# Optimization experiments

Measured on AMD Instinct MI355X. Metric: run time of the kernel, lower is better.

Reference implementation:

```python
import jax, jax.numpy as jnp
import numpy as np

T = 100000   # total firing-model timesteps (undefined global `time` in source; chosen)
WARM = 200   # warm-start rows (time_fomer = data[0:200, :])
N = 69       # neurons
EPS = 1e-5   # torch BatchNorm default eps


def _conv_same(x, w):
    # torch conv2d_same_padding with k=4, stride=1: F.pad([0,1,0,1]) then conv padding=1
    # => asymmetric SAME padding (1,2) on each spatial dim, output H,W preserved.
    return jax.lax.conv_general_dilated(
        x, w, (1, 1), [(1, 2), (1, 2)],
        dimension_numbers=('NCHW', 'OIHW', 'NCHW'))


def _up2(x):
    # nearest-neighbor upsample x2 (F.upsample(size=2*H, mode='nearest'))
    return jnp.repeat(jnp.repeat(x, 2, axis=2), 2, axis=3)


def _bn(x, g, b):
    # BatchNorm2d in training mode: batch statistics over (N,H,W), biased variance.
    m = x.mean(axis=(0, 2, 3), keepdims=True)
    v = x.var(axis=(0, 2, 3), keepdims=True)
    return (x - m) * jax.lax.rsqrt(v + EPS) * g[None, :, None, None] + b[None, :, None, None]


def _forward(x, start_part, W_in, b_in, w1, w2, w3, w4, w5,
             g1, be1, g2, be2, g3, be3, g4, be4, W_d2, b_d2):
    h = x @ W_in.T + b_in                                   # (1, 12800)
    h = h.reshape(-1, 512, 5, 5)
    h = jax.nn.relu(_bn(_conv_same(_up2(h), w1), g1, be1))  # (1,512,10,10)
    h = jax.nn.relu(_bn(_conv_same(_up2(h), w2), g2, be2))  # (1,256,20,20)
    h = jax.nn.relu(_bn(_conv_same(_up2(h), w3), g3, be3))  # (1,128,40,40)
    h = jax.nn.relu(_bn(_conv_same(_up2(h), w4), g4, be4))  # (1,64,80,80)
    h = jnp.tanh(_conv_same(h, w5))                         # (1,1,80,80)
    h = h.reshape(80 * 80) @ W_d2.T + b_d2                  # (4761,)
    w = h.reshape(N, N)                                     # coupling matrix

    # spiking recurrence: spike[t, i] = -spike[t-1, i] + tanh(sum_j w[j, i] * spike[t-1, j])
    def step(prev, _):
        new = -prev + jnp.tanh(prev @ w)                    # (69,)
        return new, new

    _, rows = jax.lax.scan(step, start_part[-1], None, length=T - WARM)
    return rows[None]                                       # (1, T-200, 69)


def setup_inputs() -> dict:
    key = jax.random.key(0)
    ks = jax.random.split(key, 9)
    f32 = jnp.float32
    return {
        'x': jax.random.normal(ks[0], (1, 2048), f32),
        'start_part': jax.random.normal(ks[1], (WARM, N), f32),
        'W_in': jax.random.normal(ks[2], (12800, 2048), f32) * (2048.0 ** -0.5),
        'b_in': jnp.zeros((12800,), f32),
        'w1': jax.random.uniform(ks[3], (512, 512, 4, 4), f32),
        'w2': jax.random.uniform(ks[4], (256, 512, 4, 4), f32),
        'w3': jax.random.uniform(ks[5], (128, 256, 4, 4), f32),
        'w4': jax.random.uniform(ks[6], (64, 128, 4, 4), f32),
        'w5': jax.random.uniform(ks[7], (1, 64, 4, 4), f32),
        'g1': jnp.ones((512,), f32), 'be1': jnp.zeros((512,), f32),
        'g2': jnp.ones((256,), f32), 'be2': jnp.zeros((256,), f32),
        'g3': jnp.ones((128,), f32), 'be3': jnp.zeros((128,), f32),
        'g4': jnp.ones((64,), f32), 'be4': jnp.zeros((64,), f32),
        'W_d2': jax.random.normal(ks[8], (4761, 6400), f32) * (6400.0 ** -0.5),
        'b_d2': jnp.zeros((4761,), f32),
    }


def reference(x, start_part, W_in, b_in, w1, w2, w3, w4, w5,
              g1, be1, g2, be2, g3, be3, g4, be4, W_d2, b_d2):
    return _forward(x, start_part, W_in, b_in, w1, w2, w3, w4, w5,
                    g1, be1, g2, be2, g3, be3, g4, be4, W_d2, b_d2)
```

## Files before the change

### kernel.cpp

```cpp
#include <hip/hip_runtime.h>
#include <cstddef>
#include <cstdint>

__global__ void fc1_k(const float* __restrict__ W, const float* __restrict__ x,
                      const float* __restrict__ b, float* __restrict__ y,
                      int rows, int cols) {
  int wave = threadIdx.x >> 6, lane = threadIdx.x & 63;
  int r = blockIdx.x * 4 + wave;
  if (r >= rows) return;
  const float* wp = W + (size_t)r * cols;
  float s = 0.f;
  for (int j = lane; j < cols; j += 64) s = fmaf(wp[j], x[j], s);
  for (int o = 32; o; o >>= 1) s += __shfl_down(s, o);
  if (lane == 0) y[r] = s + b[r];
}

template <int UP>
__global__ void conv_k(const float* __restrict__ in, const float* __restrict__ wt,
                       float* __restrict__ out, int Cin, int Cout, int OH, int OW,
                       int Hin, int Win) {
  int idx = blockIdx.x * blockDim.x + threadIdx.x;
  int total = Cout * OH * OW;
  if (idx >= total) return;
  int ox = idx % OW;
  int tt = idx / OW;
  int oy = tt % OH;
  int co = tt / OH;
  const float* wco = wt + (size_t)co * Cin * 16;
  float acc = 0.f;
  for (int ci = 0; ci < Cin; ++ci) {
    const float* ip = in + (size_t)ci * Hin * Win;
    const float* wp = wco + ci * 16;
#pragma unroll
    for (int ky = 0; ky < 4; ++ky) {
      int iy = oy - 1 + ky;
      if ((unsigned)iy >= (unsigned)OH) continue;
      int sy = UP ? (iy >> 1) : iy;
      const float* iprow = ip + sy * Win;
#pragma unroll
      for (int kx = 0; kx < 4; ++kx) {
        int ix = ox - 1 + kx;
        if ((unsigned)ix >= (unsigned)OW) continue;
        int sx = UP ? (ix >> 1) : ix;
        acc = fmaf(iprow[sx], wp[ky * 4 + kx], acc);
      }
    }
  }
  out[idx] = acc;
}

__global__ void stats_k(const float* __restrict__ x, float* __restrict__ mean,
                        float* __restrict__ rstd, int HW) {
  int c = blockIdx.x;
  const float* p = x + (size_t)c * HW;
  double s = 0.0, s2 = 0.0;
  for (int i = threadIdx.x; i < HW; i += blockDim.x) {
    float v = p[i];
    s += v;
    s2 += (double)v * (double)v;
  }
  for (int o = 32; o; o >>= 1) {
    s += __shfl_down(s, o);
    s2 += __shfl_down(s2, o);
  }
  __shared__ double sh[2][4];
  int wv = threadIdx.x >> 6, ln = threadIdx.x & 63;
  if (ln == 0) { sh[0][wv] = s; sh[1][wv] = s2; }
  __syncthreads();
  if (threadIdx.x == 0) {
    double S = 0, S2 = 0;
    int nw = blockDim.x >> 6;
    for (int w = 0; w < nw; ++w) { S += sh[0][w]; S2 += sh[1][w]; }
    double m = S / HW;
    double v = S2 / HW - m * m;
    if (v < 0) v = 0;
    mean[c] = (float)m;
    rstd[c] = rsqrtf((float)v + 1e-5f);
  }
}

__global__ void bnrelu_k(float* __restrict__ x, const float* __restrict__ mean,
                         const float* __restrict__ rstd, const float* __restrict__ g,
                         const float* __restrict__ be, int HW, int total) {
  int idx = blockIdx.x * blockDim.x + threadIdx.x;
  if (idx >= total) return;
  int c = idx / HW;
  float v = (x[idx] - mean[c]) * rstd[c] * g[c] + be[c];
  x[idx] = v > 0.f ? v : 0.f;
}

__global__ void tanh_k(float* __restrict__ x, int n) {
  int i = blockIdx.x * blockDim.x + threadIdx.x;
  if (i < n) x[i] = tanhf(x[i]);
}

__global__ void fc2_k(const float* __restrict__ W, const float* __restrict__ h,
                      const float* __restrict__ b, float* __restrict__ y, int cols) {
  int r = blockIdx.x;
  const float* wp = W + (size_t)r * cols;
  float s = 0.f;
  for (int j = threadIdx.x; j < cols; j += blockDim.x) s = fmaf(wp[j], h[j], s);
  for (int o = 32; o; o >>= 1) s += __shfl_down(s, o);
  __shared__ float sh[4];
  int wv = threadIdx.x >> 6, ln = threadIdx.x & 63;
  if (ln == 0) sh[wv] = s;
  __syncthreads();
  if (threadIdx.x == 0) y[r] = sh[0] + sh[1] + sh[2] + sh[3] + b[r];
}

__global__ __launch_bounds__(320, 1) void scan_k(const float* __restrict__ wmat,
                                                 const float* __restrict__ start,
                                                 float* __restrict__ out, int steps) {
  const int t = threadIdx.x;
  const int i = t >> 2;
  const int k = t & 3;
  float wr[20];
#pragma unroll
  for (int m = 0; m < 20; ++m) {
    int j = 20 * k + m;
    wr[m] = (i < 69 && j < 69) ? wmat[(size_t)j * 69 + i] : 0.f;
  }
  __shared__ __align__(16) float pbuf[2][80];
  if (t < 80) {
    pbuf[0][t] = (t < 69) ? start[t] : 0.f;
    pbuf[1][t] = 0.f;
  }
  __syncthreads();
  int p = 0;
  for (int step = 0; step < steps; ++step) {
    const float* pv = pbuf[p];
    const float4* q = reinterpret_cast<const float4*>(pv) + 5 * k;
    float4 q0 = q[0], q1 = q[1], q2 = q[2], q3 = q[3], q4 = q[4];
    float prev_i = pv[i];
    float a0 = q0.x * wr[0];
    float a1 = q0.y * wr[1];
    float a2 = q0.z * wr[2];
    float a3 = q0.w * wr[3];
    a0 = fmaf(q1.x, wr[4], a0);
    a1 = fmaf(q1.y, wr[5], a1);
    a2 = fmaf(q1.z, wr[6], a2);
    a3 = fmaf(q1.w, wr[7], a3);
    a0 = fmaf(q2.x, wr[8], a0);
    a1 = fmaf(q2.y, wr[9], a1);
    a2 = fmaf(q2.z, wr[10], a2);
    a3 = fmaf(q2.w, wr[11], a3);
    a0 = fmaf(q3.x, wr[12], a0);
    a1 = fmaf(q3.y, wr[13], a1);
    a2 = fmaf(q3.z, wr[14], a2);
    a3 = fmaf(q3.w, wr[15], a3);
    a0 = fmaf(q4.x, wr[16], a0);
    a1 = fmaf(q4.y, wr[17], a1);
    a2 = fmaf(q4.z, wr[18], a2);
    a3 = fmaf(q4.w, wr[19], a3);
    float s = (a0 + a1) + (a2 + a3);
    s += __shfl_xor(s, 1);
    s += __shfl_xor(s, 2);
    float e = __expf(2.f * s);
    float th = 1.f - __fdividef(2.f, e + 1.f);
    float nv = th - prev_i;
    if (i < 69) {
      if (k == 0) pbuf[p ^ 1][i] = nv;
      else if (k == 1) out[(size_t)step * 69 + i] = nv;
    }
    __syncthreads();
    p ^= 1;
  }
}

extern "C" void kernel_launch(void* const* d_in, const int* in_sizes, int n_in,
                              void* d_out, int out_size, void* d_ws, size_t ws_size,
                              hipStream_t stream) {
  const float* x    = (const float*)d_in[0];
  const float* strt = (const float*)d_in[1];
  const float* W_in = (const float*)d_in[2];
  const float* b_in = (const float*)d_in[3];
  const float* w1   = (const float*)d_in[4];
  const float* w2   = (const float*)d_in[5];
  const float* w3   = (const float*)d_in[6];
  const float* w4   = (const float*)d_in[7];
  const float* w5   = (const float*)d_in[8];
  const float* g1   = (const float*)d_in[9];
  const float* be1  = (const float*)d_in[10];
  const float* g2   = (const float*)d_in[11];
  const float* be2  = (const float*)d_in[12];
  const float* g3   = (const float*)d_in[13];
  const float* be3  = (const float*)d_in[14];
  const float* g4   = (const float*)d_in[15];
  const float* be4  = (const float*)d_in[16];
  const float* W_d2 = (const float*)d_in[17];
  const float* b_d2 = (const float*)d_in[18];
  float* out = (float*)d_out;

  float* ws   = (float*)d_ws;
  float* fc1  = ws;
  float* A    = ws + 16384;
  float* B    = A + 204800;
  float* mean = B + 409600;
  float* rstd = mean + 512;
  float* wmat = rstd + 512;

  fc1_k<<<12800 / 4, 256, 0, stream>>>(W_in, x, b_in, fc1, 12800, 2048);

  conv_k<1><<<(512 * 100 + 255) / 256, 256, 0, stream>>>(fc1, w1, A, 512, 512, 10, 10, 5, 5);
  stats_k<<<512, 256, 0, stream>>>(A, mean, rstd, 100);
  bnrelu_k<<<(51200 + 255) / 256, 256, 0, stream>>>(A, mean, rstd, g1, be1, 100, 51200);

  conv_k<1><<<(256 * 400 + 255) / 256, 256, 0, stream>>>(A, w2, B, 512, 256, 20, 20, 10, 10);
  stats_k<<<256, 256, 0, stream>>>(B, mean, rstd, 400);
  bnrelu_k<<<(102400 + 255) / 256, 256, 0, stream>>>(B, mean, rstd, g2, be2, 400, 102400);

  conv_k<1><<<(128 * 1600 + 255) / 256, 256, 0, stream>>>(B, w3, A, 256, 128, 40, 40, 20, 20);
  stats_k<<<128, 256, 0, stream>>>(A, mean, rstd, 1600);
  bnrelu_k<<<(204800 + 255) / 256, 256, 0, stream>>>(A, mean, rstd, g3, be3, 1600, 204800);

  conv_k<1><<<(64 * 6400 + 255) / 256, 256, 0, stream>>>(A, w4, B, 128, 64, 80, 80, 40, 40);
  stats_k<<<64, 256, 0, stream>>>(B, mean, rstd, 6400);
  bnrelu_k<<<(409600 + 255) / 256, 256, 0, stream>>>(B, mean, rstd, g4, be4, 6400, 409600);

  conv_k<0><<<(6400 + 255) / 256, 256, 0, stream>>>(B, w5, A, 64, 1, 80, 80, 80, 80);
  tanh_k<<<(6400 + 255) / 256, 256, 0, stream>>>(A, 6400);

  fc2_k<<<4761, 256, 0, stream>>>(W_d2, A, b_d2, wmat, 6400);

  scan_k<<<1, 320, 0, stream>>>(wmat, strt + 199 * 69, out, 99800);
}
```

Measured before the change: 36.70 ms.

## Run spiking recurrence in a single wavefront using readlane broadcasts

The sequential scan moves from a 320-thread block, which exchanged state through shared memory and needed __syncthreads each step, to a single 64-lane wavefront. Each lane holds two columns of the coupling matrix in registers (138 floats). The previous state vector is broadcast with readlane, so the per-step barrier, LDS round trip and cross-lane reduction are gone. The cost is 138 serial FMAs per lane per step instead of about 20, plus high register pressure that could spill.

```diff
diff --git a/kernel.cpp b/kernel.cpp
--- a/kernel.cpp
+++ b/kernel.cpp
@@ -108,62 +108,53 @@
   if (threadIdx.x == 0) y[r] = sh[0] + sh[1] + sh[2] + sh[3] + b[r];
 }
 
-__global__ __launch_bounds__(320, 1) void scan_k(const float* __restrict__ wmat,
-                                                 const float* __restrict__ start,
-                                                 float* __restrict__ out, int steps) {
-  const int t = threadIdx.x;
-  const int i = t >> 2;
-  const int k = t & 3;
-  float wr[20];
-#pragma unroll
-  for (int m = 0; m < 20; ++m) {
-    int j = 20 * k + m;
-    wr[m] = (i < 69 && j < 69) ? wmat[(size_t)j * 69 + i] : 0.f;
-  }
-  __shared__ __align__(16) float pbuf[2][80];
-  if (t < 80) {
-    pbuf[0][t] = (t < 69) ? start[t] : 0.f;
-    pbuf[1][t] = 0.f;
-  }
-  __syncthreads();
-  int p = 0;
+__global__ __launch_bounds__(64, 1) void scan_k(const float* __restrict__ wmat,
+                                                const float* __restrict__ start,
+                                                float* __restrict__ out, int steps) {
+  const int l = threadIdx.x;
+  const int sec = (l < 5) ? 64 + l : l;
+
+  float2 wp[69];
+#pragma unroll
+  for (int j = 0; j < 69; ++j) {
+    wp[j].x = wmat[j * 69 + l];
+    wp[j].y = wmat[j * 69 + sec];
+  }
+
+  float2 p;
+  p.x = start[l];
+  p.y = start[sec];
+
   for (int step = 0; step < steps; ++step) {
-    const float* pv = pbuf[p];
-    const float4* q = reinterpret_cast<const float4*>(pv) + 5 * k;
-    float4 q0 = q[0], q1 = q[1], q2 = q[2], q3 = q[3], q4 = q[4];
-    float prev_i = pv[i];
-    float a0 = q0.x * wr[0];
-    float a1 = q0.y * wr[1];
-    float a2 = q0.z * wr[2];
-    float a3 = q0.w * wr[3];
-    a0 = fmaf(q1.x, wr[4], a0);
-    a1 = fmaf(q1.y, wr[5], a1);
-    a2 = fmaf(q1.z, wr[6], a2);
-    a3 = fmaf(q1.w, wr[7], a3);
-    a0 = fmaf(q2.x, wr[8], a0);
-    a1 = fmaf(q2.y, wr[9], a1);
-    a2 = fmaf(q2.z, wr[10], a2);
-    a3 = fmaf(q2.w, wr[11], a3);
-    a0 = fmaf(q3.x, wr[12], a0);
-    a1 = fmaf(q3.y, wr[13], a1);
-    a2 = fmaf(q3.z, wr[14], a2);
-    a3 = fmaf(q3.w, wr[15], a3);
-    a0 = fmaf(q4.x, wr[16], a0);
-    a1 = fmaf(q4.y, wr[17], a1);
-    a2 = fmaf(q4.z, wr[18], a2);
-    a3 = fmaf(q4.w, wr[19], a3);
-    float s = (a0 + a1) + (a2 + a3);
-    s += __shfl_xor(s, 1);
-    s += __shfl_xor(s, 2);
-    float e = __expf(2.f * s);
-    float th = 1.f - __fdividef(2.f, e + 1.f);
-    float nv = th - prev_i;
-    if (i < 69) {
-      if (k == 0) pbuf[p ^ 1][i] = nv;
-      else if (k == 1) out[(size_t)step * 69 + i] = nv;
+    float2 acc;
+    acc.x = 0.f;
+    acc.y = 0.f;
+#pragma unroll
+    for (int j = 0; j < 64; ++j) {
+      float bj = __uint_as_float(
+          __builtin_amdgcn_readlane(__float_as_uint(p.x), j));
+      acc.x = fmaf(bj, wp[j].x, acc.x);
+      acc.y = fmaf(bj, wp[j].y, acc.y);
     }
-    __syncthreads();
-    p ^= 1;
+#pragma unroll
+    for (int j = 64; j < 69; ++j) {
+      float bj = __uint_as_float(
+          __builtin_amdgcn_readlane(__float_as_uint(p.y), j - 64));
+      acc.x = fmaf(bj, wp[j].x, acc.x);
+      acc.y = fmaf(bj, wp[j].y, acc.y);
+    }
+    float e0 = __expf(2.f * acc.x);
+    float t0 = fmaf(-2.f, __builtin_amdgcn_rcpf(e0 + 1.f), 1.f);
+    float e1 = __expf(2.f * acc.y);
+    float t1 = fmaf(-2.f, __builtin_amdgcn_rcpf(e1 + 1.f), 1.f);
+
+    float2 np;
+    np.x = t0 - p.x;
+    np.y = t1 - p.y;
+
+    out[(size_t)step * 69 + l] = np.x;
+    if (l < 5) out[(size_t)step * 69 + 64 + l] = np.y;
+    p = np;
   }
 }
 
@@ -222,5 +213,5 @@
 
   fc2_k<<<4761, 256, 0, stream>>>(W_d2, A, b_d2, wmat, 6400);
 
-  scan_k<<<1, 320, 0, stream>>>(wmat, strt + 199 * 69, out, 99800);
-}
+  scan_k<<<1, 64, 0, stream>>>(wmat, strt + 199 * 69, out, 99800);
+}
```

After: 66.34 ms. 1.81x slower.
